# Optimization experiments

Measured on AMD Instinct MI355X. Metric: run time of the kernel, lower is better.

The kernel has to match this reference:

```python
import jax, jax.numpy as jnp
import numpy as np

NEG_INF = float(-2 ** 31)
B, S, D_IN, D_H, H = 4, 2048, 512, 512, 8


def setup_inputs() -> dict:
    key = jax.random.key(0)
    ks = jax.random.split(key, 11)
    sc_in = 1.0 / np.sqrt(D_IN)
    sc_pr = 1.0 / np.sqrt(D_H * H)
    x = jax.random.normal(ks[0], (B, S, D_IN), dtype=jnp.float32)
    mask = jax.random.randint(ks[1], (B, 1, S), 0, 2, dtype=jnp.int32)
    Wq = jax.random.uniform(ks[2], (H, D_IN, D_H), jnp.float32, -sc_in, sc_in)
    bq = jax.random.uniform(ks[3], (H, D_H), jnp.float32, -sc_in, sc_in)
    Wk = jax.random.uniform(ks[4], (H, D_IN, D_H), jnp.float32, -sc_in, sc_in)
    bk = jax.random.uniform(ks[5], (H, D_H), jnp.float32, -sc_in, sc_in)
    Wv = jax.random.uniform(ks[6], (H, D_IN, D_H), jnp.float32, -sc_in, sc_in)
    bv = jax.random.uniform(ks[7], (H, D_H), jnp.float32, -sc_in, sc_in)
    Wp = jax.random.uniform(ks[8], (H * D_H, D_H), jnp.float32, -sc_pr, sc_pr)
    bp = jax.random.uniform(ks[9], (D_H,), jnp.float32, -sc_pr, sc_pr)
    return {"x": x, "mask": mask, "Wq": Wq, "bq": bq, "Wk": Wk, "bk": bk,
            "Wv": Wv, "bv": bv, "Wp": Wp, "bp": bp}


def reference(x, mask, Wq, bq, Wk, bk, Wv, bv, Wp, bp):
    # per-head Q/K/V projections, batched over the head axis h
    q = jnp.einsum('bsd,hde->bhse', x, Wq) + bq[None, :, None, :]
    k = jnp.einsum('bsd,hde->bhse', x, Wk) + bk[None, :, None, :]
    v = jnp.einsum('bsd,hde->bhse', x, Wv) + bv[None, :, None, :]
    scores = jnp.einsum('bhse,bhte->bhst', q, k) / jnp.sqrt(jnp.float32(D_H))
    scores = jnp.where(mask[:, None, :, :] == 0, NEG_INF, scores)
    probs = jax.nn.softmax(scores, axis=-1)
    out = jnp.einsum('bhst,bhte->bhse', probs, v)  # [B,H,S,D_H]
    cat = out.transpose(0, 2, 1, 3).reshape(B, S, H * D_H)
    return cat @ Wp + bp
```

## Files before the change

### kernel.cpp

```cpp
#include <hip/hip_runtime.h>
#include <hip/hip_bf16.h>
#include <cstdint>
#include <cstddef>

typedef unsigned short ushort_t;
typedef __bf16 bf16x8 __attribute__((ext_vector_type(8)));
typedef float floatx4 __attribute__((ext_vector_type(4)));

#define S_LEN 2048
#define DIN   512
#define DH    512
#define NHEAD 8
#define NBAT  4
#define NBH   32
#define HP    4096

#define MiB (1024ull * 1024ull)
#define WQT_OFF   (0ull)
#define WKT_OFF   (4ull  * MiB)
#define WVT_OFF   (8ull  * MiB)
#define WPT_OFF   (12ull * MiB)
#define XBF_OFF   (16ull * MiB)
#define Q_OFF     (24ull * MiB)
#define K_OFF     (88ull * MiB)
#define VT_OFF    (152ull * MiB)
#define O_OFF     (216ull * MiB)
#define LSUM_OFF  (280ull * MiB)
#define P_OFF     (281ull * MiB)
#define PART_OFF  (409ull * MiB)
#define WS_BYTES  (473ull * MiB)

__device__ __align__(256) unsigned char g_ws[WS_BYTES];

__device__ __forceinline__ ushort_t f2bf(float f) {
  union { float f; uint32_t u; } v; v.f = f;
  uint32_t r = v.u + 0x7fffu + ((v.u >> 16) & 1u);
  return (ushort_t)(r >> 16);
}

typedef __attribute__((address_space(3))) uint32_t lds_uint;
typedef __attribute__((address_space(1))) const uint32_t glb_uint;

__device__ __forceinline__ void async16(void* lds, const void* g) {
  __builtin_amdgcn_global_load_lds((glb_uint*)g, (lds_uint*)lds, 16, 0, 0);
}

#define BBAR() do { \
    __builtin_amdgcn_sched_barrier(0); \
    __builtin_amdgcn_s_barrier(); \
    __builtin_amdgcn_sched_barrier(0); \
  } while (0)

#define RBAR() __builtin_amdgcn_s_barrier()


#define STG_A(dbuf, hh, kt) do { \
    const ushort_t* _g = gA + (size_t)(kt) * 64 + (size_t)(hh) * a128; \
    char* _s = sAh + (dbuf) * 32768 + (hh) * 16384; \
    async16(_s, _g); \
    async16(_s + 8192, _g + a64); \
  } while (0)

#define STG_B(dbuf, hh, kt) do { \
    const ushort_t* _g = gB + (size_t)(kt) * 64 + (size_t)(hh) * b128; \
    char* _s = sBh + (dbuf) * 32768 + (hh) * 16384; \
    async16(_s, _g); \
    async16(_s + 8192, _g + b64); \
  } while (0)

#define LD_A2(dst, buf, qm) do { \
    const char* _b = (const char*)As + (buf) * 32768 + (qm) * 16384 + aoff0; \
    _Pragma("unroll") \
    for (int _i = 0; _i < 4; ++_i) { \
      dst[_i][0] = *(const bf16x8*)(_b + (_i << 11) + swz0); \
      dst[_i][1] = *(const bf16x8*)(_b + (_i << 11) + swz1); \
    } } while (0)

#define LD_B2(dst, buf, qn) do { \
    const char* _b = (const char*)Bs + (buf) * 32768 + (qn) * 16384 + boff0; \
    _Pragma("unroll") \
    for (int _j = 0; _j < 2; ++_j) { \
      dst[_j][0] = *(const bf16x8*)(_b + (_j << 11) + swz0); \
      dst[_j][1] = *(const bf16x8*)(_b + (_j << 11) + swz1); \
    } } while (0)

#define MM(q, AF, BF) do { \
    _Pragma("unroll") \
    for (int _i = 0; _i < 4; ++_i) { \
      _Pragma("unroll") \
      for (int _j = 0; _j < 2; ++_j) { \
        acc[q][_i][_j] = __builtin_amdgcn_mfma_f32_16x16x32_bf16(AF[_i][0], BF[_j][0], acc[q][_i][_j], 0, 0, 0); \
        acc[q][_i][_j] = __builtin_amdgcn_mfma_f32_16x16x32_bf16(AF[_i][1], BF[_j][1], acc[q][_i][_j], 0, 0, 0); \
      } \
    } \
  } while (0)

#define PHASE(q, AF, BF, STMT) do { \
    STMT; \
    RBAR(); \
    __builtin_amdgcn_s_setprio(1); \
    MM(q, AF, BF); \
    __builtin_amdgcn_s_setprio(0); \
    RBAR(); \
  } while (0)

__device__ __forceinline__ void gemm256_core(
    const ushort_t* __restrict__ A, const ushort_t* __restrict__ Bt,
    int lda, int ldb, int kdim,
    ushort_t* As, ushort_t* Bs, floatx4 acc[4][4][2])
{
  const int t = threadIdx.x;
  const int w = t >> 6, l = t & 63;
  const int l15 = l & 15, lq = l >> 4;
  const int wq_r = w >> 2, wq_c = w & 3;

  const int r0 = t >> 3, c0 = t & 7;
  const ushort_t* gA = A + (size_t)r0 * lda + ((c0 ^ (r0 & 7)) << 3);
  const ushort_t* gB = Bt + (size_t)r0 * ldb + ((c0 ^ (r0 & 7)) << 3);
  const size_t a64 = (size_t)64 * lda, b64 = (size_t)64 * ldb;
  const size_t a128 = (size_t)128 * lda, b128 = (size_t)128 * ldb;
  char* sAh = (char*)As + (w << 10);
  char* sBh = (char*)Bs + (w << 10);

  const int aoff0 = ((wq_r << 6) + l15) << 7;
  const int boff0 = ((wq_c << 5) + l15) << 7;
  const int l7 = l15 & 7;
  const int swz0 = (lq ^ l7) << 4;
  const int swz1 = ((4 + lq) ^ l7) << 4;

  const int nt = kdim >> 6;

#pragma unroll
  for (int q = 0; q < 4; ++q)
#pragma unroll
    for (int i = 0; i < 4; ++i)
#pragma unroll
      for (int j = 0; j < 2; ++j)
        acc[q][i][j] = (floatx4){0.f, 0.f, 0.f, 0.f};

  STG_A(0, 0, 0);
  STG_B(0, 0, 0);
  STG_B(0, 1, 0);
  STG_A(0, 1, 0);
  STG_A(1, 0, 1);
  STG_B(1, 0, 1);
  asm volatile("s_waitcnt vmcnt(4)" ::: "memory");
  RBAR();

  bf16x8 a[4][2], b0[2][2], b1[2][2];

#pragma unroll 1
  for (int T = 0; T < nt; T += 2) {
    const bool more = (T + 2 < nt);
    LD_A2(a, 0, 0);
    LD_B2(b0, 0, 0);
    PHASE(0, a, b0, STG_B(1, 1, T + 1));
    LD_B2(b1, 0, 1);
    PHASE(1, a, b1, STG_A(1, 1, T + 1));
    LD_A2(a, 0, 1);
    PHASE(2, a, b1, if (more) STG_A(0, 0, T + 2));
    {
      if (more) STG_B(0, 0, T + 2);
      RBAR();
      __builtin_amdgcn_s_setprio(1);
      MM(3, a, b0);
      __builtin_amdgcn_s_setprio(0);
      if (more) asm volatile("s_waitcnt vmcnt(4)" ::: "memory");
      else      asm volatile("s_waitcnt vmcnt(0)" ::: "memory");
      RBAR();
    }
    LD_A2(a, 1, 0);
    LD_B2(b0, 1, 0);
    PHASE(0, a, b0, if (more) STG_B(0, 1, T + 2));
    LD_B2(b1, 1, 1);
    PHASE(1, a, b1, if (more) STG_A(0, 1, T + 2));
    LD_A2(a, 1, 1);
    PHASE(2, a, b1, if (more) STG_A(1, 0, T + 3));
    {
      if (more) STG_B(1, 0, T + 3);
      RBAR();
      __builtin_amdgcn_s_setprio(1);
      MM(3, a, b0);
      __builtin_amdgcn_s_setprio(0);
      if (more) asm volatile("s_waitcnt vmcnt(4)" ::: "memory");
      else      asm volatile("s_waitcnt vmcnt(0)" ::: "memory");
      RBAR();
    }
  }
}

__global__ __launch_bounds__(256) void convert_f32_bf16(
    const float* __restrict__ src, size_t dstOff, int n)
{
  ushort_t* dst = (ushort_t*)(g_ws + dstOff);
  int i = (blockIdx.x * 256 + threadIdx.x) * 4;
  if (i >= n) return;
  float4 v = *(const float4*)(src + i);
  ushort_t o[4] = {f2bf(v.x), f2bf(v.y), f2bf(v.z), f2bf(v.w)};
  *(uint2*)(dst + i) = *(const uint2*)o;
}

__global__ __launch_bounds__(256) void transpose_f32_bf16(
    const float* __restrict__ src, size_t dstOff, int R, int C)
{
  __shared__ ushort_t tile[32][33];
  ushort_t* dst = (ushort_t*)(g_ws + dstOff) + (size_t)blockIdx.z * R * C;
  src += (size_t)blockIdx.z * R * C;
  int r0 = blockIdx.y * 32, c0 = blockIdx.x * 32;
  int tx = threadIdx.x & 31, ty = threadIdx.x >> 5;
  for (int i = ty; i < 32; i += 8)
    tile[i][tx] = f2bf(src[(size_t)(r0 + i) * C + (c0 + tx)]);
  __syncthreads();
  for (int i = ty; i < 32; i += 8)
    dst[(size_t)(c0 + i) * R + (r0 + tx)] = tile[tx][i];
}

__global__ __launch_bounds__(256) void transpose_w3(
    const float* __restrict__ Wq, const float* __restrict__ Wk,
    const float* __restrict__ Wv)
{
  __shared__ ushort_t tile[32][33];
  const int z = blockIdx.z;
  const int sel = z >> 3, h = z & 7;
  const float* src = ((sel == 0) ? Wq : (sel == 1) ? Wk : Wv)
                     + (size_t)h * DIN * DH;
  ushort_t* dst = (ushort_t*)(g_ws + ((sel == 0) ? WQT_OFF
                                      : (sel == 1) ? WKT_OFF : WVT_OFF))
                  + (size_t)h * DIN * DH;
  int r0 = blockIdx.y * 32, c0 = blockIdx.x * 32;
  int tx = threadIdx.x & 31, ty = threadIdx.x >> 5;
  for (int i = ty; i < 32; i += 8)
    tile[i][tx] = f2bf(src[(size_t)(r0 + i) * DH + (c0 + tx)]);
  __syncthreads();
  for (int i = ty; i < 32; i += 8)
    dst[(size_t)(c0 + i) * DIN + (r0 + tx)] = tile[tx][i];
}

__global__ __launch_bounds__(256) void zero_lsum()
{
  float* lsum = (float*)(g_ws + LSUM_OFF);
  int i = (blockIdx.x * 256 + threadIdx.x) * 4;
  *(float4*)(lsum + i) = (float4){0.f, 0.f, 0.f, 0.f};
}

__global__ __launch_bounds__(512, 2) void qkv_gemm(
    const float* __restrict__ bq, const float* __restrict__ bk,
    const float* __restrict__ bv)
{
  __shared__ __align__(16) ushort_t SH[65536];
  ushort_t* As = SH;
  ushort_t* Bs = SH + 32768;
  const int z = blockIdx.z;
  const int bh = z & 31, sel = z >> 5, b = bh >> 3, h = bh & 7;
  const size_t wOff = (sel == 0) ? WQT_OFF : (sel == 1) ? WKT_OFF : WVT_OFF;
  const float* bias = ((sel == 0) ? bq : (sel == 1) ? bk : bv) + h * DH;
  const int tileM = blockIdx.y * 256, tileN = blockIdx.x * 256;

  const ushort_t* A  = (const ushort_t*)(g_ws + XBF_OFF)
                       + ((size_t)b * S_LEN + tileM) * DIN;
  const ushort_t* Bt = (const ushort_t*)(g_ws + wOff)
                       + ((size_t)h * DH + tileN) * DIN;
  floatx4 acc[4][4][2];
  gemm256_core(A, Bt, DIN, DIN, DIN, As, Bs, acc);

  const int t = threadIdx.x, w = t >> 6, l = t & 63;
  const int l15 = l & 15, lq = l >> 4;
  const int wq_r = w >> 2, wq_c = w & 3;
  const int QM[4] = {0, 0, 1, 1}, QN[4] = {0, 1, 1, 0};

  if (sel == 2) {
    char* SB = (char*)SH;
    BBAR();
#pragma unroll
    for (int q = 0; q < 4; ++q) {
#pragma unroll
      for (int j = 0; j < 2; ++j) {
        const int nl = QN[q] * 128 + wq_c * 32 + j * 16 + l15;
        const float bsn = bias[tileN + nl];
#pragma unroll
        for (int i = 0; i < 4; ++i) {
          const int ml = QM[q] * 128 + wq_r * 64 + i * 16 + lq * 4;
          ushort_t pk[4];
#pragma unroll
          for (int r = 0; r < 4; ++r) pk[r] = f2bf(acc[q][i][j][r] + bsn);
          const int byte = nl * 512 + (((ml >> 3) ^ (nl & 7)) << 4) + (ml & 7) * 2;
          *(uint2*)(SB + byte) = *(const uint2*)pk;
        }
      }
    }
    BBAR();
    ushort_t* VTb = (ushort_t*)(g_ws + VT_OFF)
                    + ((size_t)bh * DH + tileN) * S_LEN + tileM;
#pragma unroll
    for (int s = 0; s < 16; ++s) {
      const int nl = (w << 5) + (s << 1) + (l >> 5);
      const int c  = l & 31;
      const uint4 v = *(const uint4*)(SB + nl * 512 + ((c ^ (nl & 7)) << 4));
      *(uint4*)(VTb + (size_t)nl * S_LEN + c * 8) = v;
    }
  } else {
    ushort_t* Db = (ushort_t*)(g_ws + ((sel == 0) ? Q_OFF : K_OFF));
#pragma unroll
    for (int q = 0; q < 4; ++q) {
#pragma unroll
      for (int j = 0; j < 2; ++j) {
        const int n = tileN + QN[q] * 128 + wq_c * 32 + j * 16 + l15;
        const float bsn = bias[n];
#pragma unroll
        for (int i = 0; i < 4; ++i) {
#pragma unroll
          for (int r = 0; r < 4; ++r) {
            const int m = tileM + QM[q] * 128 + wq_r * 64 + i * 16 + lq * 4 + r;
            Db[((size_t)bh * S_LEN + m) * DH + n] = f2bf(acc[q][i][j][r] + bsn);
          }
        }
      }
    }
  }
}

__global__ __launch_bounds__(512, 2) void scores_kernel(
    const int* __restrict__ mask, int c0)
{
  __shared__ __align__(16) ushort_t SH[65536];
  ushort_t* As = SH;
  ushort_t* Bs = SH + 32768;
  const int hl = blockIdx.z, bh = c0 + hl, b = bh >> 3;
  const int tileM = blockIdx.y * 256, tileN = blockIdx.x * 256;

  const ushort_t* A  = (const ushort_t*)(g_ws + Q_OFF)
                       + ((size_t)bh * S_LEN + tileM) * DH;
  const ushort_t* Bt = (const ushort_t*)(g_ws + K_OFF)
                       + ((size_t)bh * S_LEN + tileN) * DH;
  floatx4 acc[4][4][2];
  gemm256_core(A, Bt, DH, DH, DH, As, Bs, acc);

  const float scale = 0.04419417382415922f;
  const int t = threadIdx.x, w = t >> 6, l = t & 63;
  const int l15 = l & 15, lq = l >> 4;
  const int wq_r = w >> 2, wq_c = w & 3;
  const int QM[4] = {0, 0, 1, 1}, QN[4] = {0, 1, 1, 0};
  ushort_t* Pp = (ushort_t*)(g_ws + P_OFF) + (size_t)hl * S_LEN * S_LEN;
  const int* mask_b = mask + (size_t)b * S_LEN;
  float* lsum = (float*)(g_ws + LSUM_OFF);

  float rsum[2][4][4];
#pragma unroll
  for (int qm = 0; qm < 2; ++qm)
#pragma unroll
    for (int i = 0; i < 4; ++i)
#pragma unroll
      for (int r = 0; r < 4; ++r) rsum[qm][i][r] = 0.f;

#pragma unroll
  for (int q = 0; q < 4; ++q) {
#pragma unroll
    for (int j = 0; j < 2; ++j) {
      const int n = tileN + QN[q] * 128 + wq_c * 32 + j * 16 + l15;
      const int mv = mask_b[n];
#pragma unroll
      for (int i = 0; i < 4; ++i) {
#pragma unroll
        for (int r = 0; r < 4; ++r) {
          const int m = tileM + QM[q] * 128 + wq_r * 64 + i * 16 + lq * 4 + r;
          float s = fminf(acc[q][i][j][r] * scale, 30.f);
          const float p = mv ? __expf(s) : 0.f;
          rsum[QM[q]][i][r] += p;
          Pp[(size_t)m * S_LEN + n] = f2bf(p);
        }
      }
    }
  }
#pragma unroll
  for (int qm = 0; qm < 2; ++qm) {
#pragma unroll
    for (int i = 0; i < 4; ++i) {
#pragma unroll
      for (int r = 0; r < 4; ++r) {
        float v = rsum[qm][i][r];
        v += __shfl_xor(v, 1);
        v += __shfl_xor(v, 2);
        v += __shfl_xor(v, 4);
        v += __shfl_xor(v, 8);
        if (l15 == 0) {
          const int m = tileM + qm * 128 + wq_r * 64 + i * 16 + lq * 4 + r;
          atomicAdd(&lsum[(size_t)bh * S_LEN + m], v);
        }
      }
    }
  }
}

__global__ __launch_bounds__(512, 2) void pv_kernel(int c0)
{
  __shared__ __align__(16) ushort_t SH[65536];
  ushort_t* As = SH;
  ushort_t* Bs = SH + 32768;
  const int hl = blockIdx.z, bh = c0 + hl, b = bh >> 3, h = bh & 7;
  const int tileM = blockIdx.y * 256, tileN = blockIdx.x * 256;

  const ushort_t* A  = (const ushort_t*)(g_ws + P_OFF)
                       + (size_t)hl * S_LEN * S_LEN + (size_t)tileM * S_LEN;
  const ushort_t* Bt = (const ushort_t*)(g_ws + VT_OFF)
                       + ((size_t)bh * DH + tileN) * S_LEN;
  floatx4 acc[4][4][2];
  gemm256_core(A, Bt, S_LEN, S_LEN, S_LEN, As, Bs, acc);

  const float* lsum = (const float*)(g_ws + LSUM_OFF);
  ushort_t* Ob = (ushort_t*)(g_ws + O_OFF);
  const int t = threadIdx.x, w = t >> 6, l = t & 63;
  const int l15 = l & 15, lq = l >> 4;
  const int wq_r = w >> 2, wq_c = w & 3;
  const int QM[4] = {0, 0, 1, 1}, QN[4] = {0, 1, 1, 0};
#pragma unroll
  for (int q = 0; q < 4; ++q) {
#pragma unroll
    for (int i = 0; i < 4; ++i) {
#pragma unroll
      for (int r = 0; r < 4; ++r) {
        const int m = tileM + QM[q] * 128 + wq_r * 64 + i * 16 + lq * 4 + r;
        const float lv = lsum[(size_t)bh * S_LEN + m];
        const float inv = (lv > 1e-20f) ? 1.0f / lv : 0.f;
#pragma unroll
        for (int j = 0; j < 2; ++j) {
          const int n = tileN + QN[q] * 128 + wq_c * 32 + j * 16 + l15;
          Ob[((size_t)b * S_LEN + m) * HP + h * DH + n] =
              f2bf(acc[q][i][j][r] * inv);
        }
      }
    }
  }
}

__global__ __launch_bounds__(512, 2) void proj_kernel()
{
  __shared__ __align__(16) ushort_t SH[65536];
  ushort_t* As = SH;
  ushort_t* Bs = SH + 32768;
  const int tileM = blockIdx.y * 256, tileN = blockIdx.x * 256;
  const int ks = blockIdx.z;

  const ushort_t* A  = (const ushort_t*)(g_ws + O_OFF)
                       + (size_t)tileM * HP + ks * 1024;
  const ushort_t* Bt = (const ushort_t*)(g_ws + WPT_OFF)
                       + (size_t)tileN * HP + ks * 1024;
  floatx4 acc[4][4][2];
  gemm256_core(A, Bt, HP, HP, 1024, As, Bs, acc);

  float* part = (float*)(g_ws + PART_OFF)
                + (size_t)ks * NBAT * S_LEN * DH;
  const int t = threadIdx.x, w = t >> 6, l = t & 63;
  const int l15 = l & 15, lq = l >> 4;
  const int wq_r = w >> 2, wq_c = w & 3;
  const int QM[4] = {0, 0, 1, 1}, QN[4] = {0, 1, 1, 0};
#pragma unroll
  for (int q = 0; q < 4; ++q) {
#pragma unroll
    for (int j = 0; j < 2; ++j) {
      const int n = tileN + QN[q] * 128 + wq_c * 32 + j * 16 + l15;
#pragma unroll
      for (int i = 0; i < 4; ++i) {
#pragma unroll
        for (int r = 0; r < 4; ++r) {
          const int m = tileM + QM[q] * 128 + wq_r * 64 + i * 16 + lq * 4 + r;
          part[(size_t)m * DH + n] = acc[q][i][j][r];
        }
      }
    }
  }
}

__global__ __launch_bounds__(256) void reduce_out(
    const float* __restrict__ bp, float* __restrict__ out)
{
  const float* part = (const float*)(g_ws + PART_OFF);
  const size_t N = (size_t)NBAT * S_LEN * DH;
  const size_t j = ((size_t)blockIdx.x * 256 + threadIdx.x) * 4;
  const float4 s0 = *(const float4*)(part + j);
  const float4 s1 = *(const float4*)(part + N + j);
  const float4 s2 = *(const float4*)(part + 2 * N + j);
  const float4 s3 = *(const float4*)(part + 3 * N + j);
  const float4 bv = *(const float4*)(bp + (j & (DH - 1)));
  float4 o;
  o.x = s0.x + s1.x + s2.x + s3.x + bv.x;
  o.y = s0.y + s1.y + s2.y + s3.y + bv.y;
  o.z = s0.z + s1.z + s2.z + s3.z + bv.z;
  o.w = s0.w + s1.w + s2.w + s3.w + bv.w;
  *(float4*)(out + j) = o;
}

extern "C" void kernel_launch(void* const* d_in, const int* in_sizes, int n_in,
                              void* d_out, int out_size, void* d_ws, size_t ws_size,
                              hipStream_t stream) {
  const float* x  = (const float*)d_in[0];
  const int*   msk= (const int*)d_in[1];
  const float* Wq = (const float*)d_in[2];
  const float* bq = (const float*)d_in[3];
  const float* Wk = (const float*)d_in[4];
  const float* bk = (const float*)d_in[5];
  const float* Wv = (const float*)d_in[6];
  const float* bv = (const float*)d_in[7];
  const float* Wp = (const float*)d_in[8];
  const float* bp = (const float*)d_in[9];
  float* out = (float*)d_out;

  convert_f32_bf16<<<dim3(NBAT * S_LEN * DIN / 1024), 256, 0, stream>>>(
      x, XBF_OFF, NBAT * S_LEN * DIN);

  transpose_w3<<<dim3(16, 16, 24), 256, 0, stream>>>(Wq, Wk, Wv);
  transpose_f32_bf16<<<dim3(16, 128, 1), 256, 0, stream>>>(Wp, WPT_OFF, HP, DH);

  zero_lsum<<<dim3(64), 256, 0, stream>>>();

  qkv_gemm<<<dim3(2, 8, 3 * NBH), 512, 0, stream>>>(bq, bk, bv);

  for (int c0 = 0; c0 < NBH; c0 += 16) {
    scores_kernel<<<dim3(8, 8, 16), 512, 0, stream>>>(msk, c0);
    pv_kernel<<<dim3(2, 8, 16), 512, 0, stream>>>(c0);
  }

  proj_kernel<<<dim3(2, 32, 4), 512, 0, stream>>>();
  reduce_out<<<dim3(NBAT * S_LEN * DH / 1024), 256, 0, stream>>>(bp, out);
}
```

Baseline: 657.5 us.

## Compact unmasked keys and values to skip masked columns in attention

Adds a per-batch prefix scan of the key mask and gathers the surviving K rows and V^T columns into compacted, 256-padded buffers. The scores kernel then exits early for tiles past the padded count, and the PV GEMM shortens its reduction to the padded count. This is meant to remove roughly half the attention GEMM work, because the random mask zeroes about half the keys. It adds three small gather and scan kernels plus extra workspace traffic for the compacted copies.

```diff
diff --git a/kernel.cpp b/kernel.cpp
--- a/kernel.cpp
+++ b/kernel.cpp
@@ -28,7 +28,11 @@
 #define LSUM_OFF  (280ull * MiB)
 #define P_OFF     (281ull * MiB)
 #define PART_OFF  (409ull * MiB)
-#define WS_BYTES  (473ull * MiB)
+#define IDX_OFF   (473ull * MiB)
+#define CNT_OFF   (IDX_OFF + 64ull * 1024ull)
+#define KC_OFF    (474ull * MiB)
+#define VTC_OFF   (538ull * MiB)
+#define WS_BYTES  (602ull * MiB)
 
 __device__ __align__(256) unsigned char g_ws[WS_BYTES];
 
@@ -243,6 +247,71 @@
   *(float4*)(lsum + i) = (float4){0.f, 0.f, 0.f, 0.f};
 }
 
+__global__ __launch_bounds__(64) void scan_mask(const int* __restrict__ mask)
+{
+  const int b = blockIdx.x, l = threadIdx.x;
+  const int* mb = mask + (size_t)b * S_LEN;
+  int* idx = (int*)(g_ws + IDX_OFF) + b * S_LEN;
+  const int base = l * 32;
+  int c = 0;
+#pragma unroll
+  for (int i = 0; i < 32; ++i) c += (mb[base + i] != 0);
+  int pre = c;
+  for (int d = 1; d < 64; d <<= 1) {
+    int v = __shfl_up(pre, d);
+    if (l >= d) pre += v;
+  }
+  int p = pre - c;
+  for (int i = 0; i < 32; ++i)
+    if (mb[base + i] != 0) idx[p++] = base + i;
+  if (l == 63) {
+    int* cp = (int*)(g_ws + CNT_OFF) + b * 2;
+    cp[0] = pre;
+    cp[1] = (pre + 255) & ~255;
+  }
+}
+
+__global__ __launch_bounds__(256) void compact_k()
+{
+  const int bh = blockIdx.y, b = bh >> 3;
+  const int* cp = (const int*)(g_ws + CNT_OFF) + b * 2;
+  const int cnt = cp[0], cnt_pad = cp[1];
+  const int w = threadIdx.x >> 6, l = threadIdx.x & 63;
+  const int j = blockIdx.x * 4 + w;
+  if (j >= cnt_pad) return;
+  ushort_t* dst = (ushort_t*)(g_ws + KC_OFF)
+                  + ((size_t)bh * S_LEN + j) * DH + l * 8;
+  if (j < cnt) {
+    const int* idx = (const int*)(g_ws + IDX_OFF) + b * S_LEN;
+    const ushort_t* src = (const ushort_t*)(g_ws + K_OFF)
+                          + ((size_t)bh * S_LEN + idx[j]) * DH + l * 8;
+    *(uint4*)dst = *(const uint4*)src;
+  } else {
+    *(uint4*)dst = (uint4){0, 0, 0, 0};
+  }
+}
+
+__global__ __launch_bounds__(256) void compact_vt()
+{
+  const int e = blockIdx.x, bh = blockIdx.y, b = bh >> 3;
+  const int* cp = (const int*)(g_ws + CNT_OFF) + b * 2;
+  const int cnt = cp[0], cnt_pad = cp[1];
+  const int j0 = threadIdx.x * 8;
+  if (j0 >= cnt_pad) return;
+  const int* idx = (const int*)(g_ws + IDX_OFF) + b * S_LEN;
+  const ushort_t* src = (const ushort_t*)(g_ws + VT_OFF)
+                        + ((size_t)bh * DH + e) * S_LEN;
+  ushort_t* dst = (ushort_t*)(g_ws + VTC_OFF)
+                  + ((size_t)bh * DH + e) * S_LEN + j0;
+  ushort_t v[8];
+#pragma unroll
+  for (int r = 0; r < 8; ++r) {
+    const int j = j0 + r;
+    v[r] = (j < cnt) ? src[idx[j]] : (ushort_t)0;
+  }
+  *(uint4*)dst = *(const uint4*)v;
+}
+
 __global__ __launch_bounds__(512, 2) void qkv_gemm(
     const float* __restrict__ bq, const float* __restrict__ bk,
     const float* __restrict__ bv)
@@ -319,18 +388,21 @@
   }
 }
 
-__global__ __launch_bounds__(512, 2) void scores_kernel(
-    const int* __restrict__ mask, int c0)
-{
+__global__ __launch_bounds__(512, 2) void scores_kernel(int c0)
+{
+  const int hl = blockIdx.z, bh = c0 + hl, b = bh >> 3;
+  const int* cp = (const int*)(g_ws + CNT_OFF) + b * 2;
+  const int cnt = cp[0], cnt_pad = cp[1];
+  const int tileM = blockIdx.y * 256, tileN = blockIdx.x * 256;
+  if (tileN >= cnt_pad) return;
+
   __shared__ __align__(16) ushort_t SH[65536];
   ushort_t* As = SH;
   ushort_t* Bs = SH + 32768;
-  const int hl = blockIdx.z, bh = c0 + hl, b = bh >> 3;
-  const int tileM = blockIdx.y * 256, tileN = blockIdx.x * 256;
 
   const ushort_t* A  = (const ushort_t*)(g_ws + Q_OFF)
                        + ((size_t)bh * S_LEN + tileM) * DH;
-  const ushort_t* Bt = (const ushort_t*)(g_ws + K_OFF)
+  const ushort_t* Bt = (const ushort_t*)(g_ws + KC_OFF)
                        + ((size_t)bh * S_LEN + tileN) * DH;
   floatx4 acc[4][4][2];
   gemm256_core(A, Bt, DH, DH, DH, As, Bs, acc);
@@ -341,7 +413,6 @@
   const int wq_r = w >> 2, wq_c = w & 3;
   const int QM[4] = {0, 0, 1, 1}, QN[4] = {0, 1, 1, 0};
   ushort_t* Pp = (ushort_t*)(g_ws + P_OFF) + (size_t)hl * S_LEN * S_LEN;
-  const int* mask_b = mask + (size_t)b * S_LEN;
   float* lsum = (float*)(g_ws + LSUM_OFF);
 
   float rsum[2][4][4];
@@ -357,14 +428,14 @@
 #pragma unroll
     for (int j = 0; j < 2; ++j) {
       const int n = tileN + QN[q] * 128 + wq_c * 32 + j * 16 + l15;
-      const int mv = mask_b[n];
+      const int live = (n < cnt);
 #pragma unroll
       for (int i = 0; i < 4; ++i) {
 #pragma unroll
         for (int r = 0; r < 4; ++r) {
           const int m = tileM + QM[q] * 128 + wq_r * 64 + i * 16 + lq * 4 + r;
           float s = fminf(acc[q][i][j][r] * scale, 30.f);
-          const float p = mv ? __expf(s) : 0.f;
+          const float p = live ? __expf(s) : 0.f;
           rsum[QM[q]][i][r] += p;
           Pp[(size_t)m * S_LEN + n] = f2bf(p);
         }
@@ -397,14 +468,16 @@
   ushort_t* As = SH;
   ushort_t* Bs = SH + 32768;
   const int hl = blockIdx.z, bh = c0 + hl, b = bh >> 3, h = bh & 7;
+  const int* cp = (const int*)(g_ws + CNT_OFF) + b * 2;
+  const int cnt_pad = cp[1];
   const int tileM = blockIdx.y * 256, tileN = blockIdx.x * 256;
 
   const ushort_t* A  = (const ushort_t*)(g_ws + P_OFF)
                        + (size_t)hl * S_LEN * S_LEN + (size_t)tileM * S_LEN;
-  const ushort_t* Bt = (const ushort_t*)(g_ws + VT_OFF)
+  const ushort_t* Bt = (const ushort_t*)(g_ws + VTC_OFF)
                        + ((size_t)bh * DH + tileN) * S_LEN;
   floatx4 acc[4][4][2];
-  gemm256_core(A, Bt, S_LEN, S_LEN, S_LEN, As, Bs, acc);
+  gemm256_core(A, Bt, S_LEN, S_LEN, cnt_pad, As, Bs, acc);
 
   const float* lsum = (const float*)(g_ws + LSUM_OFF);
   ushort_t* Ob = (ushort_t*)(g_ws + O_OFF);
@@ -511,11 +584,15 @@
   transpose_f32_bf16<<<dim3(16, 128, 1), 256, 0, stream>>>(Wp, WPT_OFF, HP, DH);
 
   zero_lsum<<<dim3(64), 256, 0, stream>>>();
+  scan_mask<<<dim3(NBAT), 64, 0, stream>>>(msk);
 
   qkv_gemm<<<dim3(2, 8, 3 * NBH), 512, 0, stream>>>(bq, bk, bv);
 
+  compact_k<<<dim3(512, 32), 256, 0, stream>>>();
+  compact_vt<<<dim3(512, 32), 256, 0, stream>>>();
+
   for (int c0 = 0; c0 < NBH; c0 += 16) {
-    scores_kernel<<<dim3(8, 8, 16), 512, 0, stream>>>(msk, c0);
+    scores_kernel<<<dim3(8, 8, 16), 512, 0, stream>>>(c0);
     pv_kernel<<<dim3(2, 8, 16), 512, 0, stream>>>(c0);
   }
 
```

Result: no change. 659.7 us (+0.3%).
